# Kernel tuning notes

Measured on AMD Instinct MI355X. Metric: run time of the kernel, lower is better.

Reference implementation:

```python
import jax, jax.numpy as jnp
import numpy as np

B, S, D = 4, 8192, 1024
H = 16
HD = D // H          # 64
AD = 64              # approx_dim
EPS = 1e-6


def setup_inputs() -> dict:
    key = jax.random.key(0)
    ks = jax.random.split(key, 5)
    x = jax.random.normal(ks[0], (B, S, D), dtype=jnp.float32)
    # qkv_proj: Linear(D, 3*D)
    W_qkv = jax.random.normal(ks[1], (3 * D, D), dtype=jnp.float32) * (1.0 / np.sqrt(D))
    b_qkv = jnp.zeros((3 * D,), dtype=jnp.float32)
    # proj: Linear(HD, AD) with xavier_uniform init, zero bias
    limit = np.sqrt(6.0 / (HD + AD))
    W_p = jax.random.uniform(ks[2], (AD, HD), dtype=jnp.float32, minval=-limit, maxval=limit)
    b_p = jnp.zeros((AD,), dtype=jnp.float32)
    return {"x": x, "W_qkv": W_qkv, "b_qkv": b_qkv, "W_p": W_p, "b_p": b_p}


def reference(x, W_qkv, b_qkv, W_p, b_p):
    # qkv projection and split
    qkv = x @ W_qkv.T + b_qkv                      # [B,S,3D]
    Q, K, V = jnp.split(qkv, 3, axis=-1)
    # [B,S,D] -> [B,H,S,HD]
    def to_heads(t):
        return t.reshape(B, S, H, HD).transpose(0, 2, 1, 3)
    Q, K, V = to_heads(Q), to_heads(K), to_heads(V)
    # shared projection to approx dim, feature map phi(u) = sqrt(1 + u^2)
    pQ = jnp.einsum('bhsd,ad->bhsa', Q, W_p) + b_p
    pK = jnp.einsum('bhsd,ad->bhsa', K, W_p) + b_p
    phi_Q = jnp.sqrt(1.0 + pQ * pQ)                # [B,H,S,AD]
    phi_K = jnp.sqrt(1.0 + pK * pK)
    # linear attention: O(S) chained contractions
    KTV = jnp.einsum('bhsa,bhsv->bhav', phi_K, V)  # [B,H,AD,HD]
    numerator = jnp.einsum('bhsa,bhav->bhsv', phi_Q, KTV)  # [B,H,S,HD]
    k_sum = phi_K.sum(axis=2)                      # [B,H,AD]
    denominator = jnp.einsum('bhsa,bha->bhs', phi_Q, k_sum)  # [B,H,S]
    head_out = numerator / (denominator[..., None] + EPS)
    # [B,H,S,HD] -> [B,S,D]
    return head_out.transpose(0, 2, 1, 3).reshape(B, S, D)
```

## Files before the change

kernel.cpp:

```cpp
#include <hip/hip_runtime.h>
#include <hip/hip_bf16.h>
#include <cstdint>

static constexpr int Bc  = 4;
static constexpr int Sc  = 8192;
static constexpr int Dc  = 1024;
static constexpr int Hc  = 16;
static constexpr int BHc = Bc * Hc;
static constexpr int Mc  = Bc * Sc;
static constexpr int N3c = 3 * Dc;
static constexpr float EPSc = 1e-6f;

using bf16x8 = __attribute__((ext_vector_type(8))) __bf16;
using f32x4  = __attribute__((ext_vector_type(4))) float;

__device__ __forceinline__ ushort f2bf(float f) {
  union { float f; uint32_t u; } v; v.f = f;
  uint32_t u = v.u;
  return (ushort)((u + 0x7fffu + ((u >> 16) & 1u)) >> 16);
}
__device__ __forceinline__ float bf2f(ushort h) {
  union { uint32_t u; float f; } v; v.u = ((uint32_t)h) << 16;
  return v.f;
}

typedef const __attribute__((address_space(1))) unsigned int* gas_u32p;
typedef __attribute__((address_space(3))) unsigned int* las_u32p;
__device__ __forceinline__ void gld_lds16(const void* g, void* l) {
  __builtin_amdgcn_global_load_lds((gas_u32p)g, (las_u32p)l, 16, 0, 0);
}

__global__ __launch_bounds__(256) void prep_k(const float* __restrict__ x,
                                              ushort* __restrict__ xb,
                                              const float* __restrict__ Wq,
                                              const float* __restrict__ Wp,
                                              const float* __restrict__ bq,
                                              const float* __restrict__ bp,
                                              ushort* __restrict__ W3b,
                                              float* __restrict__ bias3) {
  const int t = threadIdx.x;
  if (blockIdx.x < 2048) {
    const int n4 = Mc * Dc / 4;
    for (int i = blockIdx.x * 256 + t; i < n4; i += 2048 * 256) {
      float4 v = reinterpret_cast<const float4*>(x)[i];
      ushort4 o; o.x = f2bf(v.x); o.y = f2bf(v.y); o.z = f2bf(v.z); o.w = f2bf(v.w);
      reinterpret_cast<ushort4*>(xb)[i] = o;
    }
    return;
  }
  const int bx = blockIdx.x - 2048;
  const int p = bx >> 4, h = bx & 15;
  if (p == 2) {
    const int base = 2048 + h * 64;
    for (int li = t; li < 64 * 256; li += 256) {
      int r = li >> 8, c4 = (li & 255) * 4;
      float4 v = *reinterpret_cast<const float4*>(&Wq[(size_t)(base + r) * 1024 + c4]);
      ushort4 o; o.x = f2bf(v.x); o.y = f2bf(v.y); o.z = f2bf(v.z); o.w = f2bf(v.w);
      *reinterpret_cast<ushort4*>(&W3b[(size_t)(base + r) * 1024 + c4]) = o;
    }
    if (t < 64) bias3[base + t] = bq[base + t];
    return;
  }
  __shared__ ushort Ws[64 * 64];
  __shared__ ushort Tq[256 * 64];
  const int rbase = p * 1024 + h * 64;
  for (int li = t; li < 64 * 16; li += 256) {
    int a = li >> 4, h4 = (li & 15) * 4;
    float4 v = *reinterpret_cast<const float4*>(&Wp[a * 64 + h4]);
    ushort4 o; o.x = f2bf(v.x); o.y = f2bf(v.y); o.z = f2bf(v.z); o.w = f2bf(v.w);
    *reinterpret_cast<ushort4*>(&Ws[a * 64 + h4]) = o;
  }
  if (t < 64) {
    float s = bp[t];
    for (int hd = 0; hd < 64; ++hd) s += Wp[t * 64 + hd] * bq[rbase + hd];
    bias3[rbase + t] = s;
  }
  const int w = t >> 6, lane = t & 63, lr = lane & 15, kg = lane >> 4;
  for (int dt = 0; dt < 4; ++dt) {
    __syncthreads();
    for (int li = t; li < 64 * 64; li += 256) {
      int hd = li >> 6, d4 = (li & 63) * 4;
      float4 v = *reinterpret_cast<const float4*>(&Wq[(size_t)(rbase + hd) * 1024 + dt * 256 + d4]);
      Tq[(d4 + 0) * 64 + hd] = f2bf(v.x);
      Tq[(d4 + 1) * 64 + hd] = f2bf(v.y);
      Tq[(d4 + 2) * 64 + hd] = f2bf(v.z);
      Tq[(d4 + 3) * 64 + hd] = f2bf(v.w);
    }
    __syncthreads();
    f32x4 acc[4][4];
#pragma unroll
    for (int i = 0; i < 4; i++)
#pragma unroll
      for (int j = 0; j < 4; j++) acc[i][j] = (f32x4){0.f, 0.f, 0.f, 0.f};
#pragma unroll
    for (int kk = 0; kk < 2; ++kk) {
      bf16x8 af[4], bfr[4];
#pragma unroll
      for (int i = 0; i < 4; i++)
        af[i] = *reinterpret_cast<const bf16x8*>(&Ws[(i * 16 + lr) * 64 + kk * 32 + kg * 8]);
#pragma unroll
      for (int j = 0; j < 4; j++)
        bfr[j] = *reinterpret_cast<const bf16x8*>(&Tq[(w * 64 + j * 16 + lr) * 64 + kk * 32 + kg * 8]);
#pragma unroll
      for (int i = 0; i < 4; i++)
#pragma unroll
        for (int j = 0; j < 4; j++)
          acc[i][j] = __builtin_amdgcn_mfma_f32_16x16x32_bf16(af[i], bfr[j], acc[i][j], 0, 0, 0);
    }
#pragma unroll
    for (int i = 0; i < 4; i++)
#pragma unroll
      for (int j = 0; j < 4; j++)
#pragma unroll
        for (int r = 0; r < 4; r++)
          W3b[(size_t)(rbase + i * 16 + kg * 4 + r) * 1024 + dt * 256 + w * 64 + j * 16 + lr] =
              f2bf(acc[i][j][r]);
  }
}

__global__ __launch_bounds__(512, 2) void gemm_pipe_k(const ushort* __restrict__ xb,
                                                      const ushort* __restrict__ W3b,
                                                      const float* __restrict__ bias3,
                                                      ushort* __restrict__ Qb,
                                                      ushort* __restrict__ KTb,
                                                      ushort* __restrict__ VTb) {
  __shared__ __align__(16) ushort As[4 * 8192];
  __shared__ __align__(16) ushort Bs[4 * 8192];
  const int t = threadIdx.x, wave = t >> 6, lane = t & 63;
  const int lr = lane & 15, kg = lane >> 4;
  const int wr = wave >> 2, wc = wave & 3;

  const int flat = blockIdx.x;
  const int swz  = (flat & 7) * 192 + (flat >> 3);
  const int n0 = (swz % 12) * 256;
  const int m0 = (swz / 12) * 256;

  const int srow = t >> 2;
  const int sg   = (t & 3) ^ ((t >> 3) & 3);
  const int swb  = wave * 512;

  auto STAGE = [&](int tile, int buf) {
    const int kt = tile * 32;
#pragma unroll
    for (int is = 0; is < 2; ++is) {
      gld_lds16(xb  + (size_t)(m0 + is * 128 + srow) * 1024 + kt + sg * 8,
                As + buf * 8192 + is * 4096 + swb);
      gld_lds16(W3b + (size_t)(n0 + is * 128 + srow) * 1024 + kt + sg * 8,
                Bs + buf * 8192 + is * 4096 + swb);
    }
  };

  f32x4 acc[8][4];
#pragma unroll
  for (int f = 0; f < 8; f++)
#pragma unroll
    for (int j = 0; j < 4; j++) acc[f][j] = (f32x4){0.f, 0.f, 0.f, 0.f};

  const int cp = (kg ^ ((lr >> 1) & 3)) * 8;
  const ushort* Ard = As + (wr * 128 + lr) * 32 + cp;
  const ushort* Brd = Bs + (wc * 64 + lr) * 32 + cp;

  auto COMPUTE = [&](int buf) {
    bf16x8 af[8], bfr[4];
    const ushort* Ab = Ard + buf * 8192;
    const ushort* Bb = Brd + buf * 8192;
#pragma unroll
    for (int f = 0; f < 8; f++) af[f] = *reinterpret_cast<const bf16x8*>(Ab + f * 512);
#pragma unroll
    for (int j = 0; j < 4; j++) bfr[j] = *reinterpret_cast<const bf16x8*>(Bb + j * 512);
    __builtin_amdgcn_s_setprio(1);
#pragma unroll
    for (int f = 0; f < 8; f++)
#pragma unroll
      for (int j = 0; j < 4; j++)
        acc[f][j] = __builtin_amdgcn_mfma_f32_16x16x32_bf16(af[f], bfr[j], acc[f][j], 0, 0, 0);
    __builtin_amdgcn_s_setprio(0);
  };

  STAGE(0, 0);
  STAGE(1, 1);
  STAGE(2, 2);
  asm volatile("s_waitcnt vmcnt(8)" ::: "memory");
  __builtin_amdgcn_s_barrier();

#pragma unroll 1
  for (int i = 0; i < 7; ++i) {
    const int tb = i * 4;
#pragma unroll
    for (int j = 0; j < 4; ++j) {
      STAGE(tb + j + 3, (j + 3) & 3);
      COMPUTE(j);
      asm volatile("s_waitcnt vmcnt(8)" ::: "memory");
      __builtin_amdgcn_s_barrier();
    }
  }
  STAGE(31, 3);
  COMPUTE(0);
  asm volatile("s_waitcnt vmcnt(8)" ::: "memory");
  __builtin_amdgcn_s_barrier();
  COMPUTE(1);
  asm volatile("s_waitcnt vmcnt(4)" ::: "memory");
  __builtin_amdgcn_s_barrier();
  COMPUTE(2);
  asm volatile("s_waitcnt vmcnt(0)" ::: "memory");
  __builtin_amdgcn_s_barrier();
  COMPUTE(3);

  const int n0w  = n0 + wc * 64;
  const int part = n0w >> 10;
  const int h    = (n0w & 1023) >> 6;
  const int bq   = m0 >> 13;
  const int s_base = (m0 & 8191) + wr * 128;
  float bias[4];
#pragma unroll
  for (int j = 0; j < 4; j++) bias[j] = bias3[n0w + j * 16 + lr];

  if (part == 0) {
    ushort* dst = Qb + ((size_t)(bq * Hc + h)) * Sc * 64;
#pragma unroll
    for (int f = 0; f < 8; f++)
#pragma unroll
      for (int j = 0; j < 4; j++)
#pragma unroll
        for (int r = 0; r < 4; r++) {
          float p = acc[f][j][r] + bias[j];
          dst[(size_t)(s_base + f * 16 + kg * 4 + r) * 64 + j * 16 + lr] =
              f2bf(sqrtf(1.f + p * p));
        }
  } else {
    ushort* dst = ((part == 1) ? KTb : VTb) + ((size_t)(bq * Hc + h)) * 64 * Sc;
#pragma unroll
    for (int f = 0; f < 8; f++) {
      const int s = s_base + f * 16 + kg * 4;
#pragma unroll
      for (int j = 0; j < 4; j++) {
        ushort4 o;
        if (part == 1) {
#pragma unroll
          for (int r = 0; r < 4; r++) {
            float p = acc[f][j][r] + bias[j];
            (&o.x)[r] = f2bf(sqrtf(1.f + p * p));
          }
        } else {
#pragma unroll
          for (int r = 0; r < 4; r++) (&o.x)[r] = f2bf(acc[f][j][r] + bias[j]);
        }
        *reinterpret_cast<ushort4*>(&dst[(size_t)(j * 16 + lr) * Sc + s]) = o;
      }
    }
  }
}

__global__ __launch_bounds__(256, 2) void ktv_part_k(const ushort* __restrict__ KT,
                                                     const ushort* __restrict__ VT,
                                                     float* __restrict__ KTVp,
                                                     float* __restrict__ ksump) {
  __shared__ __align__(16) ushort Ks[2 * 8192];
  __shared__ __align__(16) ushort Vs[2 * 8192];
  const int t = threadIdx.x, chunk = blockIdx.x, bh = blockIdx.y;
  const int wave = t >> 6, lane = t & 63, lr = lane & 15, kg = lane >> 4;
  const size_t hb = (size_t)bh * 64 * Sc;
  const int s0 = chunk * 1024;

  f32x4 acc[4];
  f32x4 acc_ks;
#pragma unroll
  for (int j = 0; j < 4; j++) acc[j] = (f32x4){0.f, 0.f, 0.f, 0.f};
  acc_ks = (f32x4){0.f, 0.f, 0.f, 0.f};

  bf16x8 ones;
#pragma unroll
  for (int e = 0; e < 8; e++) ones[e] = (__bf16)1.0f;

  const int srl = t >> 4;
  const int scc = (t & 15) ^ ((t >> 4) & 7);
  const int wb  = (t >> 6) * 512;

  auto STG = [&](int st, int buf) {
    const int sb = s0 + st * 128;
#pragma unroll
    for (int is = 0; is < 4; ++is) {
      const int row = is * 16 + srl;
      gld_lds16(KT + hb + (size_t)row * Sc + sb + scc * 8, Ks + buf * 8192 + is * 2048 + wb);
      gld_lds16(VT + hb + (size_t)row * Sc + sb + scc * 8, Vs + buf * 8192 + is * 2048 + wb);
    }
  };

  auto COMPUTE = [&](int buf) {
    const ushort* Kb = Ks + buf * 8192;
    const ushort* Vb = Vs + buf * 8192;
#pragma unroll
    for (int ks4 = 0; ks4 < 4; ++ks4) {
      const int pos = ((ks4 * 4 + kg) ^ (lr & 7)) * 8;
      bf16x8 af = *reinterpret_cast<const bf16x8*>(Kb + (wave * 16 + lr) * 128 + pos);
      acc_ks = __builtin_amdgcn_mfma_f32_16x16x32_bf16(af, ones, acc_ks, 0, 0, 0);
#pragma unroll
      for (int j = 0; j < 4; ++j) {
        bf16x8 bv = *reinterpret_cast<const bf16x8*>(Vb + (j * 16 + lr) * 128 + pos);
        acc[j] = __builtin_amdgcn_mfma_f32_16x16x32_bf16(af, bv, acc[j], 0, 0, 0);
      }
    }
  };

  STG(0, 0);
  __syncthreads();
#pragma unroll 1
  for (int st = 0; st < 8; ++st) {
    if (st < 7) STG(st + 1, (st + 1) & 1);
    COMPUTE(st & 1);
    __syncthreads();
  }

  float* outp = KTVp + ((size_t)bh * 8 + chunk) * 4096;
#pragma unroll
  for (int j = 0; j < 4; ++j)
#pragma unroll
    for (int r = 0; r < 4; ++r)
      outp[(wave * 16 + kg * 4 + r) * 64 + j * 16 + lr] = acc[j][r];
  if (lr == 0) {
#pragma unroll
    for (int r = 0; r < 4; ++r)
      ksump[((size_t)bh * 8 + chunk) * 64 + wave * 16 + kg * 4 + r] = acc_ks[r];
  }
}

__global__ __launch_bounds__(256) void ktv_red_k(const float* __restrict__ KTVp,
                                                 const float* __restrict__ ksump,
                                                 float* __restrict__ KTV,
                                                 float* __restrict__ ksum) {
  const int bh = blockIdx.x, t = threadIdx.x;
  for (int li = t; li < 4096; li += 256) {
    float s = 0.f;
    for (int c = 0; c < 8; c++) s += KTVp[((size_t)bh * 8 + c) * 4096 + li];
    KTV[(size_t)bh * 4096 + li] = s;
  }
  if (t < 64) {
    float s = 0.f;
    for (int c = 0; c < 8; c++) s += ksump[((size_t)bh * 8 + c) * 64 + t];
    ksum[bh * 64 + t] = s;
  }
}

__global__ __launch_bounds__(256) void out_k(const ushort* __restrict__ Qphi,
                                             const float* __restrict__ KTV,
                                             const float* __restrict__ ksum,
                                             float* __restrict__ out) {
  __shared__ ushort Qs[256][72];
  __shared__ ushort BT[64][72];
  __shared__ float  den[256];
  __shared__ float  kss[64];
  const int t = threadIdx.x;
  const int bh = blockIdx.y, s0 = blockIdx.x * 256;
  const ushort* qb = Qphi + (size_t)bh * Sc * 64 + (size_t)s0 * 64;

#pragma unroll
  for (int i = 0; i < 8; i++) {
    int li = i * 256 + t;
    int r = li >> 3, c8 = li & 7;
    *reinterpret_cast<uint4*>(&Qs[r][c8 * 8]) = *reinterpret_cast<const uint4*>(&qb[li * 8]);
  }
  for (int li = t; li < 4096; li += 256) {
    int a = li >> 6, v = li & 63;
    BT[v][a] = f2bf(KTV[(size_t)bh * 4096 + li]);
  }
  if (t < 64) kss[t] = ksum[bh * 64 + t];
  __syncthreads();

  {
    float d = 0.f;
    for (int a = 0; a < 64; a++) d += bf2f(Qs[t][a]) * kss[a];
    den[t] = d + EPSc;
  }
  __syncthreads();

  const int wave = t >> 6, lane = t & 63, lr = lane & 15, kg = lane >> 4;
  f32x4 acc[4][4];
#pragma unroll
  for (int i = 0; i < 4; i++)
#pragma unroll
    for (int j = 0; j < 4; j++) acc[i][j] = (f32x4){0.f, 0.f, 0.f, 0.f};

#pragma unroll
  for (int ks = 0; ks < 64; ks += 32) {
    bf16x8 af[4], bfr[4];
#pragma unroll
    for (int i = 0; i < 4; i++)
      af[i] = *reinterpret_cast<const bf16x8*>(&Qs[wave * 64 + i * 16 + lr][ks + kg * 8]);
#pragma unroll
    for (int j = 0; j < 4; j++)
      bfr[j] = *reinterpret_cast<const bf16x8*>(&BT[j * 16 + lr][ks + kg * 8]);
#pragma unroll
    for (int i = 0; i < 4; i++)
#pragma unroll
      for (int j = 0; j < 4; j++)
        acc[i][j] = __builtin_amdgcn_mfma_f32_16x16x32_bf16(af[i], bfr[j], acc[i][j], 0, 0, 0);
  }

  const int bq = bh >> 4, h = bh & 15;
#pragma unroll
  for (int i = 0; i < 4; i++) {
#pragma unroll
    for (int j = 0; j < 4; j++) {
#pragma unroll
      for (int r = 0; r < 4; r++) {
        int row = wave * 64 + i * 16 + kg * 4 + r;
        int s = s0 + row;
        int v = j * 16 + lr;
        out[((size_t)bq * Sc + s) * 1024 + h * 64 + v] = acc[i][j][r] / den[row];
      }
    }
  }
}

extern "C" void kernel_launch(void* const* d_in, const int* in_sizes, int n_in,
                              void* d_out, int out_size, void* d_ws, size_t ws_size,
                              hipStream_t stream) {
  const float* x     = (const float*)d_in[0];
  const float* W_qkv = (const float*)d_in[1];
  const float* b_qkv = (const float*)d_in[2];
  const float* W_p   = (const float*)d_in[3];
  const float* b_p   = (const float*)d_in[4];
  float* out = (float*)d_out;

  size_t off = 0;
  auto carve = [&](size_t bytes) -> void* {
    void* p = (char*)d_ws + off;
    off += (bytes + 255) & ~(size_t)255;
    return p;
  };
  const size_t headElems = (size_t)BHc * Sc * 64;
  ushort* xb    = (ushort*)carve((size_t)Mc * Dc * 2);
  ushort* Qb    = (ushort*)carve(headElems * 2);
  ushort* KTb   = (ushort*)carve(headElems * 2);
  ushort* VTb   = (ushort*)carve(headElems * 2);
  ushort* W3b   = (ushort*)carve((size_t)N3c * Dc * 2);
  float*  bias3 = (float*)carve((size_t)N3c * 4);
  float*  KTVp  = (float*)carve((size_t)BHc * 8 * 4096 * 4);
  float*  ksmp  = (float*)carve((size_t)BHc * 8 * 64 * 4);
  float*  KTV   = (float*)carve((size_t)BHc * 4096 * 4);
  float*  ksum  = (float*)carve((size_t)BHc * 64 * 4);
  (void)ws_size; (void)n_in; (void)in_sizes; (void)out_size;

  prep_k<<<2096, 256, 0, stream>>>(x, xb, W_qkv, W_p, b_qkv, b_p, W3b, bias3);
  gemm_pipe_k<<<(Mc / 256) * (N3c / 256), 512, 0, stream>>>(xb, W3b, bias3, Qb, KTb, VTb);
  ktv_part_k<<<dim3(8, BHc), 256, 0, stream>>>(KTb, VTb, KTVp, ksmp);
  ktv_red_k<<<BHc, 256, 0, stream>>>(KTVp, ksmp, KTV, ksum);
  out_k<<<dim3(Sc / 256, BHc), 256, 0, stream>>>(Qb, KTV, ksum, out);
}
```

Measured before the change: 405.3 us.

## Fuse Q projection GEMM with output contraction, skip Q intermediate buffer

Splits the QKV GEMM into a K/V GEMM that runs first and a Q GEMM that runs after the KTV reduction. The Q GEMM's epilogue applies phi, stages phi_Q in LDS, and computes the numerator via MFMA and the denominator via wave shuffles, writing the final output directly. This removes the global write and re-read of the bf16 Q tensor and the separate out_k launch. The KTV reduction now emits a transposed bf16 matrix so the fused epilogue can load it directly. The cost is a heavier GEMM epilogue whose register pressure may hurt occupancy.

```diff
diff --git a/kernel.cpp b/kernel.cpp
--- a/kernel.cpp
+++ b/kernel.cpp
@@ -118,12 +118,11 @@
   }
 }
 
-__global__ __launch_bounds__(512, 2) void gemm_pipe_k(const ushort* __restrict__ xb,
-                                                      const ushort* __restrict__ W3b,
-                                                      const float* __restrict__ bias3,
-                                                      ushort* __restrict__ Qb,
-                                                      ushort* __restrict__ KTb,
-                                                      ushort* __restrict__ VTb) {
+__global__ __launch_bounds__(512, 2) void gemm_kv_k(const ushort* __restrict__ xb,
+                                                    const ushort* __restrict__ W3b,
+                                                    const float* __restrict__ bias3,
+                                                    ushort* __restrict__ KTb,
+                                                    ushort* __restrict__ VTb) {
   __shared__ __align__(16) ushort As[4 * 8192];
   __shared__ __align__(16) ushort Bs[4 * 8192];
   const int t = threadIdx.x, wave = t >> 6, lane = t & 63;
@@ -131,9 +130,9 @@
   const int wr = wave >> 2, wc = wave & 3;
 
   const int flat = blockIdx.x;
-  const int swz  = (flat & 7) * 192 + (flat >> 3);
-  const int n0 = (swz % 12) * 256;
-  const int m0 = (swz / 12) * 256;
+  const int swz  = (flat & 7) * 128 + (flat >> 3);
+  const int n0 = 1024 + (swz % 8) * 256;
+  const int m0 = (swz / 8) * 256;
 
   const int srow = t >> 2;
   const int sg   = (t & 3) ^ ((t >> 3) & 3);
@@ -215,38 +214,24 @@
 #pragma unroll
   for (int j = 0; j < 4; j++) bias[j] = bias3[n0w + j * 16 + lr];
 
-  if (part == 0) {
-    ushort* dst = Qb + ((size_t)(bq * Hc + h)) * Sc * 64;
-#pragma unroll
-    for (int f = 0; f < 8; f++)
-#pragma unroll
-      for (int j = 0; j < 4; j++)
+  ushort* dst = ((part == 1) ? KTb : VTb) + ((size_t)(bq * Hc + h)) * 64 * Sc;
+#pragma unroll
+  for (int f = 0; f < 8; f++) {
+    const int s = s_base + f * 16 + kg * 4;
+#pragma unroll
+    for (int j = 0; j < 4; j++) {
+      ushort4 o;
+      if (part == 1) {
 #pragma unroll
         for (int r = 0; r < 4; r++) {
           float p = acc[f][j][r] + bias[j];
-          dst[(size_t)(s_base + f * 16 + kg * 4 + r) * 64 + j * 16 + lr] =
-              f2bf(sqrtf(1.f + p * p));
+          (&o.x)[r] = f2bf(sqrtf(1.f + p * p));
         }
-  } else {
-    ushort* dst = ((part == 1) ? KTb : VTb) + ((size_t)(bq * Hc + h)) * 64 * Sc;
-#pragma unroll
-    for (int f = 0; f < 8; f++) {
-      const int s = s_base + f * 16 + kg * 4;
-#pragma unroll
-      for (int j = 0; j < 4; j++) {
-        ushort4 o;
-        if (part == 1) {
-#pragma unroll
-          for (int r = 0; r < 4; r++) {
-            float p = acc[f][j][r] + bias[j];
-            (&o.x)[r] = f2bf(sqrtf(1.f + p * p));
-          }
-        } else {
-#pragma unroll
-          for (int r = 0; r < 4; r++) (&o.x)[r] = f2bf(acc[f][j][r] + bias[j]);
-        }
-        *reinterpret_cast<ushort4*>(&dst[(size_t)(j * 16 + lr) * Sc + s]) = o;
+      } else {
+#pragma unroll
+        for (int r = 0; r < 4; r++) (&o.x)[r] = f2bf(acc[f][j][r] + bias[j]);
       }
+      *reinterpret_cast<ushort4*>(&dst[(size_t)(j * 16 + lr) * Sc + s]) = o;
     }
   }
 }
@@ -326,13 +311,14 @@
 
 __global__ __launch_bounds__(256) void ktv_red_k(const float* __restrict__ KTVp,
                                                  const float* __restrict__ ksump,
-                                                 float* __restrict__ KTV,
+                                                 ushort* __restrict__ KTVTb,
                                                  float* __restrict__ ksum) {
   const int bh = blockIdx.x, t = threadIdx.x;
   for (int li = t; li < 4096; li += 256) {
+    const int v = li >> 6, a = li & 63;
     float s = 0.f;
-    for (int c = 0; c < 8; c++) s += KTVp[((size_t)bh * 8 + c) * 4096 + li];
-    KTV[(size_t)bh * 4096 + li] = s;
+    for (int c = 0; c < 8; c++) s += KTVp[((size_t)bh * 8 + c) * 4096 + a * 64 + v];
+    KTVTb[(size_t)bh * 4096 + li] = f2bf(s);
   }
   if (t < 64) {
     float s = 0.f;
@@ -341,74 +327,168 @@
   }
 }
 
-__global__ __launch_bounds__(256) void out_k(const ushort* __restrict__ Qphi,
-                                             const float* __restrict__ KTV,
-                                             const float* __restrict__ ksum,
-                                             float* __restrict__ out) {
-  __shared__ ushort Qs[256][72];
-  __shared__ ushort BT[64][72];
-  __shared__ float  den[256];
-  __shared__ float  kss[64];
-  const int t = threadIdx.x;
-  const int bh = blockIdx.y, s0 = blockIdx.x * 256;
-  const ushort* qb = Qphi + (size_t)bh * Sc * 64 + (size_t)s0 * 64;
-
-#pragma unroll
-  for (int i = 0; i < 8; i++) {
-    int li = i * 256 + t;
-    int r = li >> 3, c8 = li & 7;
-    *reinterpret_cast<uint4*>(&Qs[r][c8 * 8]) = *reinterpret_cast<const uint4*>(&qb[li * 8]);
-  }
-  for (int li = t; li < 4096; li += 256) {
-    int a = li >> 6, v = li & 63;
-    BT[v][a] = f2bf(KTV[(size_t)bh * 4096 + li]);
-  }
-  if (t < 64) kss[t] = ksum[bh * 64 + t];
+__global__ __launch_bounds__(512, 2) void gemm_q_k(const ushort* __restrict__ xb,
+                                                   const ushort* __restrict__ W3b,
+                                                   const float* __restrict__ bias3,
+                                                   const ushort* __restrict__ KTVTb,
+                                                   const float* __restrict__ ksum,
+                                                   float* __restrict__ out) {
+  __shared__ __align__(16) ushort As[4 * 8192];
+  __shared__ __align__(16) ushort Bs[4 * 8192];
+  const int t = threadIdx.x, wave = t >> 6, lane = t & 63;
+  const int lr = lane & 15, kg = lane >> 4;
+  const int wr = wave >> 2, wc = wave & 3;
+
+  const int flat = blockIdx.x;
+  const int swz  = (flat & 7) * 64 + (flat >> 3);
+  const int n0 = (swz % 4) * 256;
+  const int m0 = (swz / 4) * 256;
+
+  const int srow = t >> 2;
+  const int sg   = (t & 3) ^ ((t >> 3) & 3);
+  const int swb  = wave * 512;
+
+  auto STAGE = [&](int tile, int buf) {
+    const int kt = tile * 32;
+#pragma unroll
+    for (int is = 0; is < 2; ++is) {
+      gld_lds16(xb  + (size_t)(m0 + is * 128 + srow) * 1024 + kt + sg * 8,
+                As + buf * 8192 + is * 4096 + swb);
+      gld_lds16(W3b + (size_t)(n0 + is * 128 + srow) * 1024 + kt + sg * 8,
+                Bs + buf * 8192 + is * 4096 + swb);
+    }
+  };
+
+  f32x4 acc[8][4];
+#pragma unroll
+  for (int f = 0; f < 8; f++)
+#pragma unroll
+    for (int j = 0; j < 4; j++) acc[f][j] = (f32x4){0.f, 0.f, 0.f, 0.f};
+
+  const int cp = (kg ^ ((lr >> 1) & 3)) * 8;
+  const ushort* Ard = As + (wr * 128 + lr) * 32 + cp;
+  const ushort* Brd = Bs + (wc * 64 + lr) * 32 + cp;
+
+  auto COMPUTE = [&](int buf) {
+    bf16x8 af[8], bfr[4];
+    const ushort* Ab = Ard + buf * 8192;
+    const ushort* Bb = Brd + buf * 8192;
+#pragma unroll
+    for (int f = 0; f < 8; f++) af[f] = *reinterpret_cast<const bf16x8*>(Ab + f * 512);
+#pragma unroll
+    for (int j = 0; j < 4; j++) bfr[j] = *reinterpret_cast<const bf16x8*>(Bb + j * 512);
+    __builtin_amdgcn_s_setprio(1);
+#pragma unroll
+    for (int f = 0; f < 8; f++)
+#pragma unroll
+      for (int j = 0; j < 4; j++)
+        acc[f][j] = __builtin_amdgcn_mfma_f32_16x16x32_bf16(af[f], bfr[j], acc[f][j], 0, 0, 0);
+    __builtin_amdgcn_s_setprio(0);
+  };
+
+  STAGE(0, 0);
+  STAGE(1, 1);
+  STAGE(2, 2);
+  asm volatile("s_waitcnt vmcnt(8)" ::: "memory");
+  __builtin_amdgcn_s_barrier();
+
+#pragma unroll 1
+  for (int i = 0; i < 7; ++i) {
+    const int tb = i * 4;
+#pragma unroll
+    for (int j = 0; j < 4; ++j) {
+      STAGE(tb + j + 3, (j + 3) & 3);
+      COMPUTE(j);
+      asm volatile("s_waitcnt vmcnt(8)" ::: "memory");
+      __builtin_amdgcn_s_barrier();
+    }
+  }
+  STAGE(31, 3);
+  COMPUTE(0);
+  asm volatile("s_waitcnt vmcnt(8)" ::: "memory");
+  __builtin_amdgcn_s_barrier();
+  COMPUTE(1);
+  asm volatile("s_waitcnt vmcnt(4)" ::: "memory");
+  __builtin_amdgcn_s_barrier();
+  COMPUTE(2);
+  asm volatile("s_waitcnt vmcnt(0)" ::: "memory");
+  __builtin_amdgcn_s_barrier();
+  COMPUTE(3);
+
+  const int n0w = n0 + wc * 64;
+  const int h   = n0w >> 6;
+  const int bq  = m0 >> 13;
+  const int bh  = bq * Hc + h;
+  const int s_base = (m0 & 8191) + wr * 128;
+  float bias[4];
+#pragma unroll
+  for (int j = 0; j < 4; j++) bias[j] = bias3[n0w + j * 16 + lr];
+
   __syncthreads();
-
-  {
+  ushort* ep = (wave < 4) ? (As + wave * 8192) : (Bs + (wave - 4) * 8192);
+
+#pragma unroll
+  for (int f = 0; f < 8; f++)
+#pragma unroll
+    for (int j = 0; j < 4; j++) {
+      const int g = j * 2 + (lr >> 3);
+      const int cl = lr & 7;
+#pragma unroll
+      for (int r = 0; r < 4; r++) {
+        const int row = f * 16 + kg * 4 + r;
+        float p = acc[f][j][r] + bias[j];
+        ep[row * 64 + ((g ^ (row & 7)) << 3) + cl] = f2bf(sqrtf(1.f + p * p));
+      }
+    }
+
+  bf16x8 bfr[4][2];
+#pragma unroll
+  for (int j = 0; j < 4; j++)
+#pragma unroll
+    for (int ks = 0; ks < 2; ks++)
+      bfr[j][ks] = *reinterpret_cast<const bf16x8*>(
+          &KTVTb[(size_t)bh * 4096 + (j * 16 + lr) * 64 + ks * 32 + kg * 8]);
+  float ksc[2][8];
+#pragma unroll
+  for (int ks = 0; ks < 2; ks++) {
+    float4 v0 = *reinterpret_cast<const float4*>(&ksum[bh * 64 + ks * 32 + kg * 8]);
+    float4 v1 = *reinterpret_cast<const float4*>(&ksum[bh * 64 + ks * 32 + kg * 8 + 4]);
+    ksc[ks][0] = v0.x; ksc[ks][1] = v0.y; ksc[ks][2] = v0.z; ksc[ks][3] = v0.w;
+    ksc[ks][4] = v1.x; ksc[ks][5] = v1.y; ksc[ks][6] = v1.z; ksc[ks][7] = v1.w;
+  }
+
+#pragma unroll 1
+  for (int f = 0; f < 8; f++) {
+    bf16x8 af[2];
+#pragma unroll
+    for (int ks = 0; ks < 2; ks++)
+      af[ks] = *reinterpret_cast<const bf16x8*>(
+          &ep[(f * 16 + lr) * 64 + (((ks * 4 + kg) ^ (lr & 7)) << 3)]);
     float d = 0.f;
-    for (int a = 0; a < 64; a++) d += bf2f(Qs[t][a]) * kss[a];
-    den[t] = d + EPSc;
-  }
-  __syncthreads();
-
-  const int wave = t >> 6, lane = t & 63, lr = lane & 15, kg = lane >> 4;
-  f32x4 acc[4][4];
-#pragma unroll
-  for (int i = 0; i < 4; i++)
-#pragma unroll
-    for (int j = 0; j < 4; j++) acc[i][j] = (f32x4){0.f, 0.f, 0.f, 0.f};
-
-#pragma unroll
-  for (int ks = 0; ks < 64; ks += 32) {
-    bf16x8 af[4], bfr[4];
-#pragma unroll
-    for (int i = 0; i < 4; i++)
-      af[i] = *reinterpret_cast<const bf16x8*>(&Qs[wave * 64 + i * 16 + lr][ks + kg * 8]);
+#pragma unroll
+    for (int ks = 0; ks < 2; ks++)
+#pragma unroll
+      for (int e = 0; e < 8; e++) d += (float)af[ks][e] * ksc[ks][e];
+    d += __shfl_xor(d, 16, 64);
+    d += __shfl_xor(d, 32, 64);
+    float den[4];
+#pragma unroll
+    for (int r = 0; r < 4; r++) den[r] = __shfl(d, kg * 4 + r, 64) + EPSc;
+    f32x4 nacc[4];
+#pragma unroll
+    for (int j = 0; j < 4; j++) nacc[j] = (f32x4){0.f, 0.f, 0.f, 0.f};
+#pragma unroll
+    for (int ks = 0; ks < 2; ks++)
+#pragma unroll
+      for (int j = 0; j < 4; j++)
+        nacc[j] = __builtin_amdgcn_mfma_f32_16x16x32_bf16(af[ks], bfr[j][ks], nacc[j], 0, 0, 0);
 #pragma unroll
     for (int j = 0; j < 4; j++)
-      bfr[j] = *reinterpret_cast<const bf16x8*>(&BT[j * 16 + lr][ks + kg * 8]);
-#pragma unroll
-    for (int i = 0; i < 4; i++)
-#pragma unroll
-      for (int j = 0; j < 4; j++)
-        acc[i][j] = __builtin_amdgcn_mfma_f32_16x16x32_bf16(af[i], bfr[j], acc[i][j], 0, 0, 0);
-  }
-
-  const int bq = bh >> 4, h = bh & 15;
-#pragma unroll
-  for (int i = 0; i < 4; i++) {
-#pragma unroll
-    for (int j = 0; j < 4; j++) {
 #pragma unroll
       for (int r = 0; r < 4; r++) {
-        int row = wave * 64 + i * 16 + kg * 4 + r;
-        int s = s0 + row;
-        int v = j * 16 + lr;
-        out[((size_t)bq * Sc + s) * 1024 + h * 64 + v] = acc[i][j][r] / den[row];
+        const int s = s_base + f * 16 + kg * 4 + r;
+        out[((size_t)bq * Sc + s) * 1024 + h * 64 + j * 16 + lr] = nacc[j][r] / den[r];
       }
-    }
   }
 }
 
@@ -430,20 +510,19 @@
   };
   const size_t headElems = (size_t)BHc * Sc * 64;
   ushort* xb    = (ushort*)carve((size_t)Mc * Dc * 2);
-  ushort* Qb    = (ushort*)carve(headElems * 2);
   ushort* KTb   = (ushort*)carve(headElems * 2);
   ushort* VTb   = (ushort*)carve(headElems * 2);
   ushort* W3b   = (ushort*)carve((size_t)N3c * Dc * 2);
   float*  bias3 = (float*)carve((size_t)N3c * 4);
   float*  KTVp  = (float*)carve((size_t)BHc * 8 * 4096 * 4);
   float*  ksmp  = (float*)carve((size_t)BHc * 8 * 64 * 4);
-  float*  KTV   = (float*)carve((size_t)BHc * 4096 * 4);
+  ushort* KTVTb = (ushort*)carve((size_t)BHc * 4096 * 2);
   float*  ksum  = (float*)carve((size_t)BHc * 64 * 4);
   (void)ws_size; (void)n_in; (void)in_sizes; (void)out_size;
 
   prep_k<<<2096, 256, 0, stream>>>(x, xb, W_qkv, W_p, b_qkv, b_p, W3b, bias3);
-  gemm_pipe_k<<<(Mc / 256) * (N3c / 256), 512, 0, stream>>>(xb, W3b, bias3, Qb, KTb, VTb);
+  gemm_kv_k<<<(Mc / 256) * (2048 / 256), 512, 0, stream>>>(xb, W3b, bias3, KTb, VTb);
   ktv_part_k<<<dim3(8, BHc), 256, 0, stream>>>(KTb, VTb, KTVp, ksmp);
-  ktv_red_k<<<BHc, 256, 0, stream>>>(KTVp, ksmp, KTV, ksum);
-  out_k<<<dim3(Sc / 256, BHc), 256, 0, stream>>>(Qb, KTV, ksum, out);
-}
+  ktv_red_k<<<BHc, 256, 0, stream>>>(KTVp, ksmp, KTVTb, ksum);
+  gemm_q_k<<<(Mc / 256) * (1024 / 256), 512, 0, stream>>>(xb, W3b, bias3, KTVTb, ksum, out);
+}
```

New measurement: 383.8 us (median of 3 runs). -5.3%, faster.
